# Kernel tuning notes

Measured on AMD Instinct MI355X. Metric: run time of the kernel, lower is better.

## Reference

```python
import jax, jax.numpy as jnp
import numpy as np

MARGIN = 1.0
B, D, NUM_CLASSES = 8192, 128, 10


def setup_inputs() -> dict:
    key = jax.random.key(0)
    k1, k2 = jax.random.split(key)
    embeddings = jax.random.normal(k1, (B, D), dtype=jnp.float32)
    labels = jax.random.randint(k2, (B,), 0, NUM_CLASSES, dtype=jnp.int64)
    return {"embeddings": embeddings, "labels": labels}


def reference(embeddings, labels):
    # pairwise Euclidean distances d[i, j] = sqrt(sum((e_i - e_j)^2))
    sq = jnp.sum(embeddings * embeddings, axis=-1)               # [B]
    d2 = sq[:, None] + sq[None, :] - 2.0 * (embeddings @ embeddings.T)
    dist = jnp.sqrt(jnp.maximum(d2, 0.0))                        # [B, B]

    same = labels[:, None] == labels[None, :]                    # [B, B] bool
    neg_inf = jnp.float32(-jnp.inf)
    pos_inf = jnp.float32(jnp.inf)

    # hardest positive: max distance among same-class (includes self, dist 0, harmless)
    hardest_pos = jnp.max(jnp.where(same, dist, neg_inf), axis=1)   # [B]
    # hardest negative: min distance among different-class
    hardest_neg = jnp.min(jnp.where(same, pos_inf, dist), axis=1)   # [B]

    per_anchor = jax.nn.relu(hardest_pos - hardest_neg + MARGIN)    # [B]
    # use_gt_than_zero_mean=False -> divide by batch size
    return jnp.sum(per_anchor) / per_anchor.shape[0]
```

## Files before the change

### kernel.cpp

```cpp
#include <hip/hip_runtime.h>
#include <hip/hip_bf16.h>
#include <cstdint>

#define BATCH 8192
#define DIM   128
#define MARGIN 1.0f

typedef __attribute__((ext_vector_type(8))) short short8;
typedef __attribute__((ext_vector_type(4))) float f32x4;
typedef __attribute__((ext_vector_type(4))) int   i32x4;

__device__ __forceinline__ void async_copy16(const void* g, void* lds) {
    __builtin_amdgcn_global_load_lds(
        (const __attribute__((address_space(1))) unsigned int*)g,
        (__attribute__((address_space(3))) unsigned int*)lds, 16, 0, 0);
}

__global__ __launch_bounds__(256) void bhtl_prep(
    const float* __restrict__ emb,
    __hip_bfloat16* __restrict__ Ebf,
    float* __restrict__ sq,
    unsigned* __restrict__ hp2,
    unsigned* __restrict__ hn2)
{
    const int w   = threadIdx.x >> 6;
    const int l   = threadIdx.x & 63;
    const int row = blockIdx.x * 4 + w;
    const float2 e = ((const float2*)(emb + row * DIM))[l];
    __hip_bfloat162 h2;
    h2.x = __float2bfloat16(e.x);
    h2.y = __float2bfloat16(e.y);
    ((__hip_bfloat162*)(Ebf + row * DIM))[l] = h2;
    float s = e.x * e.x + e.y * e.y;
    #pragma unroll
    for (int d = 1; d < 64; d <<= 1) s += __shfl_xor(s, d, 64);
    if (l == 0) {
        sq[row]  = s;
        hp2[row] = 0u;
        hn2[row] = 0x7F800000u;
    }
}

__global__ __launch_bounds__(128) void bhtl_main(
    const __hip_bfloat16* __restrict__ Ebf,
    const float* __restrict__ sq,
    const int* __restrict__ labels,
    unsigned* __restrict__ hp2,
    unsigned* __restrict__ hn2)
{
    __shared__ __align__(16) unsigned short B_s[2][2][4096];
    __shared__ __align__(16) float sqm[2][512];
    __shared__ __align__(16) int   labm[2][512];

    const int tid  = threadIdx.x;
    const int w    = tid >> 6;
    const int lane = tid & 63;
    const int q    = lane >> 4;
    const int ln   = lane & 15;
    const int rt   = blockIdx.x >> 4;
    const int js   = blockIdx.x & 15;
    const int rowbase = rt * 128 + w * 64;
    const int jbase   = js * 512;

    #pragma unroll
    for (int c = 0; c < 2; ++c) {
        int U = c * 64 + lane;
        async_copy16(sq     + jbase + U * 4, &sqm [w][c * 256]);
        async_copy16(labels + jbase + U * 4, &labm[w][c * 256]);
    }

    auto stageB = [&](int buf, int ch) {
        const int jb = jbase + ch * 32;
        #pragma unroll
        for (int c = 0; c < 8; ++c) {
            int U   = c * 64 + lane;
            int col = U >> 4;
            int u   = U & 15;
            int j   = u ^ (col & 7);
            async_copy16(Ebf + (size_t)(jb + col) * DIM + j * 8,
                         &B_s[w][buf][c * 64 * 8]);
        }
    };

    short8 af[4][4];
    float  sqi[4];
    int    labi[4];
    #pragma unroll
    for (int m = 0; m < 4; ++m) {
        const int row = rowbase + m * 16 + ln;
        #pragma unroll
        for (int kc = 0; kc < 4; ++kc)
            af[m][kc] = *(const short8*)(Ebf + (size_t)row * DIM + kc * 32 + q * 8);
        sqi[m]  = sq[row];
        labi[m] = labels[row];
    }

    float mp[4] = {-INFINITY, -INFINITY, -INFINITY, -INFINITY};
    float mn[4] = { INFINITY,  INFINITY,  INFINITY,  INFINITY};

    stageB(0, 0);

    #pragma unroll 2
    for (int ch = 0; ch < 16; ++ch) {
        const int buf = ch & 1;

        asm volatile("s_waitcnt vmcnt(0)" ::: "memory");

        short8 bfr[2][4];
        #pragma unroll
        for (int n = 0; n < 2; ++n)
            #pragma unroll
            for (int kc = 0; kc < 4; ++kc)
                bfr[n][kc] = *(const short8*)(
                    &B_s[w][buf][((n * 16 + ln) * 16 + (((kc * 4 + q) ^ (ln & 7)))) * 8]);
        f32x4 sqj[2];
        i32x4 labj[2];
        #pragma unroll
        for (int n = 0; n < 2; ++n) {
            sqj[n]  = *(const f32x4*)(&sqm [w][ch * 32 + n * 16 + q * 4]);
            labj[n] = *(const i32x4*)(&labm[w][ch * 32 + n * 16 + q * 4]);
        }

        if (ch < 15) stageB(buf ^ 1, ch + 1);

        f32x4 acc[4][2];
        const f32x4 zero = {0.f, 0.f, 0.f, 0.f};
        #pragma unroll
        for (int m = 0; m < 4; ++m)
            #pragma unroll
            for (int n = 0; n < 2; ++n) acc[m][n] = zero;
        #pragma unroll
        for (int kc = 0; kc < 4; ++kc)
            #pragma unroll
            for (int m = 0; m < 4; ++m)
                #pragma unroll
                for (int n = 0; n < 2; ++n)
                    acc[m][n] = __builtin_amdgcn_mfma_f32_16x16x32_bf16(
                        bfr[n][kc], af[m][kc], acc[m][n], 0, 0, 0);

        #pragma unroll
        for (int m = 0; m < 4; ++m)
            #pragma unroll
            for (int n = 0; n < 2; ++n)
                #pragma unroll
                for (int r = 0; r < 4; ++r) {
                    float val = fmaf(-2.0f, acc[m][n][r], sqj[n][r]);
                    bool same = (labi[m] == labj[n][r]);
                    mp[m] = fmaxf(mp[m], same ? val : -INFINITY);
                    mn[m] = fminf(mn[m], same ? INFINITY : val);
                }
    }

    #pragma unroll
    for (int m = 0; m < 4; ++m) {
        float a = mp[m], b = mn[m];
        a = fmaxf(a, __shfl_xor(a, 16, 64));
        a = fmaxf(a, __shfl_xor(a, 32, 64));
        b = fminf(b, __shfl_xor(b, 16, 64));
        b = fminf(b, __shfl_xor(b, 32, 64));
        if (q == 0) {
            const int row = rowbase + m * 16 + ln;
            atomicMax(&hp2[row], __float_as_uint(fmaxf(sqi[m] + a, 0.0f)));
            atomicMin(&hn2[row], __float_as_uint(fmaxf(sqi[m] + b, 0.0f)));
        }
    }
}

__global__ __launch_bounds__(1024) void bhtl_final(
    const unsigned* __restrict__ hp2,
    const unsigned* __restrict__ hn2,
    float* __restrict__ out)
{
    __shared__ float red[16];
    float sum = 0.f;
    for (int i = threadIdx.x; i < BATCH; i += 1024) {
        float hp = sqrtf(__uint_as_float(hp2[i]));
        float hn = sqrtf(__uint_as_float(hn2[i]));
        sum += fmaxf(hp - hn + MARGIN, 0.f);
    }
    #pragma unroll
    for (int d = 1; d < 64; d <<= 1) sum += __shfl_xor(sum, d, 64);
    int wv = threadIdx.x >> 6;
    if ((threadIdx.x & 63) == 0) red[wv] = sum;
    __syncthreads();
    if (threadIdx.x < 64) {
        float v = (threadIdx.x < 16) ? red[threadIdx.x] : 0.f;
        #pragma unroll
        for (int d = 1; d < 16; d <<= 1) v += __shfl_xor(v, d, 64);
        if (threadIdx.x == 0) out[0] = v / (float)BATCH;
    }
}

extern "C" void kernel_launch(void* const* d_in, const int* in_sizes, int n_in,
                              void* d_out, int out_size, void* d_ws, size_t ws_size,
                              hipStream_t stream)
{
    const float* emb    = (const float*)d_in[0];
    const int*   labels = (const int*)d_in[1];
    float*       out    = (float*)d_out;

    char* ws = (char*)d_ws;
    __hip_bfloat16* Ebf = (__hip_bfloat16*)ws;
    float*    sq   = (float*)   (ws + 2 * 1024 * 1024);
    unsigned* hp2  = (unsigned*)(ws + 2 * 1024 * 1024 + 32 * 1024);
    unsigned* hn2  = (unsigned*)(ws + 2 * 1024 * 1024 + 64 * 1024);

    bhtl_prep<<<BATCH / 4, 256, 0, stream>>>(emb, Ebf, sq, hp2, hn2);
    bhtl_main<<<1024, 128, 0, stream>>>(Ebf, sq, labels, hp2, hn2);
    bhtl_final<<<1, 1024, 0, stream>>>(hp2, hn2, out);
}
```

Baseline: 93.68 us.

## Fold label masking into GEMM via augmented one-hot dimension and triple-buffer

Each embedding gets 32 extra K columns: a one-hot label scaled by 64 in the A copy and by -64 in the B copy. After the -2x factor, same-class pairs gain a large constant offset (SEP = 8192), so the hardest positive and hardest negative both come from a plain max and min with no per-element label compare. The constant is removed before the atomics. The B tile pipeline becomes triple-buffered with 16-column chunks and partial vmcnt waits. This trades 25% more MFMA work and extra bf16 storage for cheaper epilogue VALU work, at the risk of precision loss when distances are offset by a large constant in fp32.

```diff
diff --git a/kernel.cpp b/kernel.cpp
--- a/kernel.cpp
+++ b/kernel.cpp
@@ -4,11 +4,12 @@
 
 #define BATCH 8192
 #define DIM   128
+#define KAUG  160
 #define MARGIN 1.0f
+#define SEP    8192.0f
 
 typedef __attribute__((ext_vector_type(8))) short short8;
 typedef __attribute__((ext_vector_type(4))) float f32x4;
-typedef __attribute__((ext_vector_type(4))) int   i32x4;
 
 __device__ __forceinline__ void async_copy16(const void* g, void* lds) {
     __builtin_amdgcn_global_load_lds(
@@ -18,7 +19,9 @@
 
 __global__ __launch_bounds__(256) void bhtl_prep(
     const float* __restrict__ emb,
-    __hip_bfloat16* __restrict__ Ebf,
+    const int* __restrict__ labels,
+    __hip_bfloat16* __restrict__ EbfA,
+    __hip_bfloat16* __restrict__ EbfB,
     float* __restrict__ sq,
     unsigned* __restrict__ hp2,
     unsigned* __restrict__ hn2)
@@ -30,7 +33,18 @@
     __hip_bfloat162 h2;
     h2.x = __float2bfloat16(e.x);
     h2.y = __float2bfloat16(e.y);
-    ((__hip_bfloat162*)(Ebf + row * DIM))[l] = h2;
+    ((__hip_bfloat162*)(EbfA + (size_t)row * KAUG))[l] = h2;
+    ((__hip_bfloat162*)(EbfB + (size_t)row * KAUG))[l] = h2;
+    if (l < 16) {
+        const int lab = labels[row];
+        const float a0 = (2 * l     == lab) ? 64.f : 0.f;
+        const float a1 = (2 * l + 1 == lab) ? 64.f : 0.f;
+        __hip_bfloat162 hA, hB;
+        hA.x = __float2bfloat16(a0);  hA.y = __float2bfloat16(a1);
+        hB.x = __float2bfloat16(-a0); hB.y = __float2bfloat16(-a1);
+        ((__hip_bfloat162*)(EbfA + (size_t)row * KAUG + DIM))[l] = hA;
+        ((__hip_bfloat162*)(EbfB + (size_t)row * KAUG + DIM))[l] = hB;
+    }
     float s = e.x * e.x + e.y * e.y;
     #pragma unroll
     for (int d = 1; d < 64; d <<= 1) s += __shfl_xor(s, d, 64);
@@ -42,15 +56,14 @@
 }
 
 __global__ __launch_bounds__(128) void bhtl_main(
-    const __hip_bfloat16* __restrict__ Ebf,
+    const __hip_bfloat16* __restrict__ EbfA,
+    const __hip_bfloat16* __restrict__ EbfB,
     const float* __restrict__ sq,
-    const int* __restrict__ labels,
     unsigned* __restrict__ hp2,
     unsigned* __restrict__ hn2)
 {
-    __shared__ __align__(16) unsigned short B_s[2][2][4096];
+    __shared__ __align__(16) unsigned short B_s[2][3][2560];
     __shared__ __align__(16) float sqm[2][512];
-    __shared__ __align__(16) int   labm[2][512];
 
     const int tid  = threadIdx.x;
     const int w    = tid >> 6;
@@ -62,94 +75,85 @@
     const int rowbase = rt * 128 + w * 64;
     const int jbase   = js * 512;
 
-    #pragma unroll
-    for (int c = 0; c < 2; ++c) {
-        int U = c * 64 + lane;
-        async_copy16(sq     + jbase + U * 4, &sqm [w][c * 256]);
-        async_copy16(labels + jbase + U * 4, &labm[w][c * 256]);
-    }
+    short8 af[4][5];
+    #pragma unroll
+    for (int m = 0; m < 4; ++m)
+        #pragma unroll
+        for (int kc = 0; kc < 5; ++kc) {
+            af[m][kc] = *(const short8*)(
+                EbfA + (size_t)(rowbase + m * 16 + ln) * KAUG + kc * 32 + q * 8);
+            asm("" : "+v"(af[m][kc]));
+        }
+
+    #pragma unroll
+    for (int c = 0; c < 2; ++c)
+        async_copy16(sq + jbase + (c * 64 + lane) * 4, &sqm[w][c * 256]);
+
+    asm volatile("s_waitcnt vmcnt(0)" ::: "memory");
 
     auto stageB = [&](int buf, int ch) {
-        const int jb = jbase + ch * 32;
-        #pragma unroll
-        for (int c = 0; c < 8; ++c) {
+        const int jb = jbase + ch * 16;
+        #pragma unroll
+        for (int c = 0; c < 5; ++c) {
             int U   = c * 64 + lane;
-            int col = U >> 4;
-            int u   = U & 15;
-            int j   = u ^ (col & 7);
-            async_copy16(Ebf + (size_t)(jb + col) * DIM + j * 8,
-                         &B_s[w][buf][c * 64 * 8]);
+            int col = U / 20;
+            int u   = U - col * 20;
+            int g   = (u < 16) ? (u ^ (col & 7)) : u;
+            async_copy16(EbfB + (size_t)(jb + col) * KAUG + g * 8,
+                         &B_s[w][buf][c * 512]);
         }
     };
-
-    short8 af[4][4];
-    float  sqi[4];
-    int    labi[4];
-    #pragma unroll
-    for (int m = 0; m < 4; ++m) {
-        const int row = rowbase + m * 16 + ln;
-        #pragma unroll
-        for (int kc = 0; kc < 4; ++kc)
-            af[m][kc] = *(const short8*)(Ebf + (size_t)row * DIM + kc * 32 + q * 8);
-        sqi[m]  = sq[row];
-        labi[m] = labels[row];
-    }
 
     float mp[4] = {-INFINITY, -INFINITY, -INFINITY, -INFINITY};
     float mn[4] = { INFINITY,  INFINITY,  INFINITY,  INFINITY};
 
-    stageB(0, 0);
-
-    #pragma unroll 2
-    for (int ch = 0; ch < 16; ++ch) {
-        const int buf = ch & 1;
-
-        asm volatile("s_waitcnt vmcnt(0)" ::: "memory");
-
-        short8 bfr[2][4];
-        #pragma unroll
-        for (int n = 0; n < 2; ++n)
+    auto doIter = [&](int ch, int buf, bool doStage, bool last) {
+        if (last) asm volatile("s_waitcnt vmcnt(0)" ::: "memory");
+        else      asm volatile("s_waitcnt vmcnt(5)" ::: "memory");
+
+        short8 bfr[5];
+        #pragma unroll
+        for (int kc = 0; kc < 5; ++kc) {
+            const int t    = kc * 4 + q;
+            const int unit = (kc < 4) ? (t ^ (ln & 7)) : t;
+            bfr[kc] = *(const short8*)(&B_s[w][buf][(ln * 20 + unit) * 8]);
+        }
+        f32x4 sqj = *(const f32x4*)(&sqm[w][ch * 16 + q * 4]);
+
+        if (doStage) stageB(buf == 0 ? 2 : buf - 1, ch + 2);
+
+        f32x4 acc[4];
+        const f32x4 zero = {0.f, 0.f, 0.f, 0.f};
+        #pragma unroll
+        for (int m = 0; m < 4; ++m) acc[m] = zero;
+        #pragma unroll
+        for (int kc = 0; kc < 5; ++kc)
             #pragma unroll
-            for (int kc = 0; kc < 4; ++kc)
-                bfr[n][kc] = *(const short8*)(
-                    &B_s[w][buf][((n * 16 + ln) * 16 + (((kc * 4 + q) ^ (ln & 7)))) * 8]);
-        f32x4 sqj[2];
-        i32x4 labj[2];
-        #pragma unroll
-        for (int n = 0; n < 2; ++n) {
-            sqj[n]  = *(const f32x4*)(&sqm [w][ch * 32 + n * 16 + q * 4]);
-            labj[n] = *(const i32x4*)(&labm[w][ch * 32 + n * 16 + q * 4]);
-        }
-
-        if (ch < 15) stageB(buf ^ 1, ch + 1);
-
-        f32x4 acc[4][2];
-        const f32x4 zero = {0.f, 0.f, 0.f, 0.f};
+            for (int m = 0; m < 4; ++m)
+                acc[m] = __builtin_amdgcn_mfma_f32_16x16x32_bf16(
+                    bfr[kc], af[m][kc], acc[m], 0, 0, 0);
+
         #pragma unroll
         for (int m = 0; m < 4; ++m)
             #pragma unroll
-            for (int n = 0; n < 2; ++n) acc[m][n] = zero;
-        #pragma unroll
-        for (int kc = 0; kc < 4; ++kc)
-            #pragma unroll
-            for (int m = 0; m < 4; ++m)
-                #pragma unroll
-                for (int n = 0; n < 2; ++n)
-                    acc[m][n] = __builtin_amdgcn_mfma_f32_16x16x32_bf16(
-                        bfr[n][kc], af[m][kc], acc[m][n], 0, 0, 0);
-
-        #pragma unroll
-        for (int m = 0; m < 4; ++m)
-            #pragma unroll
-            for (int n = 0; n < 2; ++n)
-                #pragma unroll
-                for (int r = 0; r < 4; ++r) {
-                    float val = fmaf(-2.0f, acc[m][n][r], sqj[n][r]);
-                    bool same = (labi[m] == labj[n][r]);
-                    mp[m] = fmaxf(mp[m], same ? val : -INFINITY);
-                    mn[m] = fminf(mn[m], same ? INFINITY : val);
-                }
-    }
+            for (int r = 0; r < 4; ++r) {
+                float val = fmaf(-2.0f, acc[m][r], sqj[r]);
+                mp[m] = fmaxf(mp[m], val);
+                mn[m] = fminf(mn[m], val);
+            }
+    };
+
+    stageB(0, 0);
+    stageB(1, 1);
+
+    #pragma unroll 1
+    for (int base = 0; base < 30; base += 3) {
+        doIter(base,     0, true, false);
+        doIter(base + 1, 1, true, false);
+        doIter(base + 2, 2, base + 2 < 30, false);
+    }
+    doIter(30, 0, false, false);
+    doIter(31, 1, false, true);
 
     #pragma unroll
     for (int m = 0; m < 4; ++m) {
@@ -160,8 +164,9 @@
         b = fminf(b, __shfl_xor(b, 32, 64));
         if (q == 0) {
             const int row = rowbase + m * 16 + ln;
-            atomicMax(&hp2[row], __float_as_uint(fmaxf(sqi[m] + a, 0.0f)));
-            atomicMin(&hn2[row], __float_as_uint(fmaxf(sqi[m] + b, 0.0f)));
+            const float sqi = sq[row];
+            atomicMax(&hp2[row], __float_as_uint(fmaxf(sqi + a - SEP, 0.0f)));
+            atomicMin(&hn2[row], __float_as_uint(fmaxf(sqi + b, 0.0f)));
         }
     }
 }
@@ -200,12 +205,13 @@
     float*       out    = (float*)d_out;
 
     char* ws = (char*)d_ws;
-    __hip_bfloat16* Ebf = (__hip_bfloat16*)ws;
-    float*    sq   = (float*)   (ws + 2 * 1024 * 1024);
-    unsigned* hp2  = (unsigned*)(ws + 2 * 1024 * 1024 + 32 * 1024);
-    unsigned* hn2  = (unsigned*)(ws + 2 * 1024 * 1024 + 64 * 1024);
-
-    bhtl_prep<<<BATCH / 4, 256, 0, stream>>>(emb, Ebf, sq, hp2, hn2);
-    bhtl_main<<<1024, 128, 0, stream>>>(Ebf, sq, labels, hp2, hn2);
+    __hip_bfloat16* EbfA = (__hip_bfloat16*)ws;
+    __hip_bfloat16* EbfB = (__hip_bfloat16*)(ws + 3  * 1024 * 1024);
+    float*    sq   = (float*)   (ws + 6 * 1024 * 1024);
+    unsigned* hp2  = (unsigned*)(ws + 6 * 1024 * 1024 + 32 * 1024);
+    unsigned* hn2  = (unsigned*)(ws + 6 * 1024 * 1024 + 64 * 1024);
+
+    bhtl_prep<<<BATCH / 4, 256, 0, stream>>>(emb, labels, EbfA, EbfB, sq, hp2, hn2);
+    bhtl_main<<<1024, 128, 0, stream>>>(EbfA, EbfB, sq, hp2, hn2);
     bhtl_final<<<1, 1024, 0, stream>>>(hp2, hn2, out);
 }
```

New measurement: 87.64 us. 6.4% less time.
